# Performance work log

Measured on AMD Instinct MI355X. Metric: run time of the kernel, lower is better.

Reference implementation:

```python
import jax, jax.numpy as jnp
import numpy as np

D_MODEL = 1024
N_HEADS = 16
D_HEAD = 64
D_FF = 4096
BATCH = 4
SEQ = 2048
EPS = 1e-05


def gelu_lean(x):
    cubic = x * x * x
    cdf = 0.5 * (1.0 + jnp.tanh(0.7978845608 * (x + 0.044715 * cubic)))
    return x * cdf


def layernorm(x, gamma, beta):
    mean = jnp.mean(x, axis=-1, keepdims=True)
    var = jnp.mean((x - mean) ** 2, axis=-1, keepdims=True)
    return gamma * ((x - mean) / jnp.sqrt(var + EPS)) + beta


def setup_inputs() -> dict:
    key = jax.random.key(0)
    ks = jax.random.split(key, 8)
    std = 0.02
    return {
        "x": jax.random.normal(ks[0], (BATCH, SEQ, D_MODEL), dtype=jnp.float32),
        "gamma1": jnp.ones((D_MODEL,), jnp.float32),
        "beta1": jnp.zeros((D_MODEL,), jnp.float32),
        "wq": std * jax.random.normal(ks[1], (N_HEADS, D_HEAD, D_MODEL), dtype=jnp.float32),
        "wk": std * jax.random.normal(ks[2], (N_HEADS, D_HEAD, D_MODEL), dtype=jnp.float32),
        "wv": std * jax.random.normal(ks[3], (N_HEADS, D_HEAD, D_MODEL), dtype=jnp.float32),
        "wo": std * jax.random.normal(ks[4], (D_MODEL, N_HEADS * D_HEAD), dtype=jnp.float32),
        "gamma2": jnp.ones((D_MODEL,), jnp.float32),
        "beta2": jnp.zeros((D_MODEL,), jnp.float32),
        "mlp_fc1": std * jax.random.normal(ks[5], (D_FF, D_MODEL), dtype=jnp.float32),
        "mlp_fc2": std * jax.random.normal(ks[6], (D_MODEL, D_FF), dtype=jnp.float32),
    }


def reference(x, gamma1, beta1, wq, wk, wv, wo, gamma2, beta2, mlp_fc1, mlp_fc2):
    n = layernorm(x, gamma1, beta1)  # [B,S,D]
    scale = jnp.sqrt(jnp.float32(D_HEAD))
    # per-head projections, vectorized over heads: [B,S,H,dh]
    q = jnp.einsum("bsd,hed->bshe", n, wq)
    k = jnp.einsum("bsd,hed->bshe", n, wk)
    v = jnp.einsum("bsd,hed->bshe", n, wv)
    scores = jnp.einsum("bqhe,bkhe->bhqk", q, k) / scale  # [B,H,S,S]
    seq = x.shape[1]
    mask = jnp.triu(jnp.ones((seq, seq), dtype=bool), k=1)
    scores = jnp.where(mask, jnp.float32(-1e9), scores)
    weights = jax.nn.softmax(scores, axis=-1)
    attn = jnp.einsum("bhqk,bkhe->bqhe", weights, v)  # [B,S,H,dh]
    concat = attn.reshape(x.shape[0], seq, N_HEADS * D_HEAD)  # head-order concat
    attn_out = concat @ wo.T
    x_resid = x + attn_out
    n2 = layernorm(x_resid, gamma2, beta2)
    hidden = gelu_lean(n2 @ mlp_fc1.T)
    mlp_out = hidden @ mlp_fc2.T
    return x_resid + mlp_out
```

## Files before the change

### kernel.cpp

```cpp
#include <hip/hip_runtime.h>
#include <hip/hip_bf16.h>

#define D_MODEL 1024
#define N_HEADS 16
#define D_HEAD  64
#define D_FF    4096
#define BATCH   4
#define SEQ     2048
#define ROWS    (BATCH*SEQ)
#define LN_EPS  1e-5f

typedef __bf16 bf16;
typedef __bf16 bf16x8 __attribute__((ext_vector_type(8)));
typedef __bf16 bf16x4 __attribute__((ext_vector_type(4)));
typedef float  f32x4  __attribute__((ext_vector_type(4)));

__device__ __forceinline__ void load16_lds(const bf16* g, bf16* l) {
#if defined(__has_builtin) && __has_builtin(__builtin_amdgcn_global_load_lds)
    __builtin_amdgcn_global_load_lds(
        (const __attribute__((address_space(1))) unsigned int*)g,
        (__attribute__((address_space(3))) unsigned int*)l,
        16, 0, 0);
#else
    const int lane = threadIdx.x & 63;
    ((bf16x8*)l)[lane] = *(const bf16x8*)g;
#endif
}

__global__ __launch_bounds__(256) void f2b4_kernel(const float* a, const float* b,
                                                   const float* c, const float* d,
                                                   bf16* oa, bf16* ob, bf16* oc, bf16* od,
                                                   int n) {
    const float* srcs[4] = {a, b, c, d};
    bf16* dsts[4] = {oa, ob, oc, od};
    const float* s = srcs[blockIdx.y];
    bf16* dst = dsts[blockIdx.y];
    int i = blockIdx.x * 256 + threadIdx.x;
    int stride = gridDim.x * 256;
    for (; i < n; i += stride) dst[i] = (bf16)s[i];
}
__global__ __launch_bounds__(256) void f2b2_kernel(const float* a, const float* b,
                                                   bf16* oa, bf16* ob, int n) {
    const float* s = blockIdx.y ? b : a;
    bf16* dst = blockIdx.y ? ob : oa;
    int i = blockIdx.x * 256 + threadIdx.x;
    int stride = gridDim.x * 256;
    for (; i < n; i += stride) dst[i] = (bf16)s[i];
}

__global__ __launch_bounds__(256) void ln_kernel(const float* __restrict__ x,
                                                 const float* __restrict__ gamma,
                                                 const float* __restrict__ beta,
                                                 bf16* __restrict__ out) {
    const int row = blockIdx.x;
    const int tid = threadIdx.x;
    const float* xr = x + (size_t)row * D_MODEL;

    float vals[4];
    float s = 0.f, ss = 0.f;
#pragma unroll
    for (int t = 0; t < 4; ++t) {
        float v = xr[tid + t * 256];
        vals[t] = v;
        s += v;
        ss += v * v;
    }
#pragma unroll
    for (int off = 32; off > 0; off >>= 1) {
        s  += __shfl_xor(s, off, 64);
        ss += __shfl_xor(ss, off, 64);
    }
    __shared__ float sbuf[4], ssbuf[4];
    const int wave = tid >> 6;
    if ((tid & 63) == 0) { sbuf[wave] = s; ssbuf[wave] = ss; }
    __syncthreads();
    s  = sbuf[0] + sbuf[1] + sbuf[2] + sbuf[3];
    ss = ssbuf[0] + ssbuf[1] + ssbuf[2] + ssbuf[3];

    const float mean = s * (1.f / D_MODEL);
    const float var  = ss * (1.f / D_MODEL) - mean * mean;
    const float inv  = rsqrtf(var + LN_EPS);

    bf16* orow = out + (size_t)row * D_MODEL;
#pragma unroll
    for (int t = 0; t < 4; ++t) {
        int c = tid + t * 256;
        orow[c] = (bf16)(gamma[c] * ((vals[t] - mean) * inv) + beta[c]);
    }
}

__device__ __forceinline__ float gelu_f(float x) {
    const float y = x * (0.7978845608f + 0.0356774081f * x * x);
    return x / (1.f + __expf(-2.f * y));
}

template <int EPI, int TN, int BK, int ORD, typename OutT>
__global__ __launch_bounds__(256) void gemm_mt(const bf16* __restrict__ A,
                                               const bf16* __restrict__ W,
                                               OutT* C,
                                               const float* ADD,
                                               bf16* VT,
                                               int M, int N, int K, int LDK) {
    constexpr int WN = TN / 64;
    constexpr int WM = 4 / WN;
    constexpr int SM = (128 / WM) / 16;

    constexpr int AB_ELEMS = 128 * BK + TN * BK;
    constexpr int TB_ELEMS = (EPI == 4) ? 4 * 64 * 72 : 0;
    constexpr int SMEM_ELEMS = AB_ELEMS > TB_ELEMS ? AB_ELEMS : TB_ELEMS;
    __shared__ __align__(16) bf16 smem[SMEM_ELEMS];
    bf16* sA   = smem;
    bf16* sB   = smem + 128 * BK;
    bf16* tbuf = smem;

    const int wave = threadIdx.x >> 6;
    const int lane = threadIdx.x & 63;
    const int quad = lane >> 4;
    const int l16  = lane & 15;
    const int wm   = wave / WN;
    const int wn   = wave % WN;

    const int nN  = N / TN;
    const int b   = blockIdx.x;
    const int xcd = b & 7;
    const int j   = b >> 3;
    int bx, band;
    if constexpr (ORD == 0) {
        bx   = j % nN;
        band = (j / nN) * 8 + xcd;
    } else {
        const int BPX = (M / 128) >> 3;
        bx   = j / BPX;
        band = (j % BPX) * 8 + xcd;
    }

    const int m0 = band * 128;
    const int n0 = bx * TN;

    f32x4 acc[SM][4] = {};

    if constexpr (BK == 32) {
        const int srow = lane >> 2;
        const int scol = (lane & 3) * 8;
        const bf16* gA0 = A + (size_t)(m0 + wave * 32 + srow) * LDK + scol;
        const bf16* gA1 = gA0 + (size_t)16 * LDK;
        bf16* lA0 = &sA[(wave * 32) * 32];
        bf16* lA1 = &sA[(wave * 32 + 16) * 32];
        const bf16* gB0 = W + (size_t)(n0 + wave * (TN / 4) + srow) * LDK + scol;
        const bf16* gB1 = gB0 + (size_t)16 * LDK;
        bf16* lB0 = &sB[(wave * (TN / 4)) * 32];
        bf16* lB1 = &sB[(wave * (TN / 4) + 16) * 32];

        for (int k0 = 0; k0 < K; k0 += 32) {
            load16_lds(gA0 + k0, lA0);
            load16_lds(gA1 + k0, lA1);
            load16_lds(gB0 + k0, lB0);
            if constexpr (TN == 128) load16_lds(gB1 + k0, lB1);
            __syncthreads();

            bf16x8 af[SM], bfr[4];
#pragma unroll
            for (int s = 0; s < SM; ++s)
                af[s] = *reinterpret_cast<const bf16x8*>(&sA[(wm * (128 / WM) + s * 16 + l16) * 32 + quad * 8]);
#pragma unroll
            for (int t = 0; t < 4; ++t)
                bfr[t] = *reinterpret_cast<const bf16x8*>(&sB[(wn * 64 + t * 16 + l16) * 32 + quad * 8]);
#pragma unroll
            for (int s = 0; s < SM; ++s)
#pragma unroll
                for (int t = 0; t < 4; ++t)
                    acc[s][t] = __builtin_amdgcn_mfma_f32_16x16x32_bf16(af[s], bfr[t], acc[s][t], 0, 0, 0);
            __syncthreads();
        }
    } else {
        const int lrow = lane >> 3;
        const int lch  = ((lane & 7) ^ lrow) * 8;
        const bf16* gA = A + (size_t)(m0 + wave * 32 + lrow) * LDK + lch;
        bf16* lA = &sA[(wave * 32) * 64];
        const bf16* gB = W + (size_t)(n0 + wave * (TN / 4) + lrow) * LDK + lch;
        bf16* lB = &sB[(wave * (TN / 4)) * 64];

        for (int k0 = 0; k0 < K; k0 += 64) {
#pragma unroll
            for (int i = 0; i < 4; ++i)
                load16_lds(gA + k0 + (size_t)(8 * i) * LDK, lA + 8 * i * 64);
#pragma unroll
            for (int i = 0; i < (TN / 4) / 8; ++i)
                load16_lds(gB + k0 + (size_t)(8 * i) * LDK, lB + 8 * i * 64);
            __syncthreads();

#pragma unroll
            for (int kk = 0; kk < 2; ++kk) {
                bf16x8 af[SM], bfr[4];
#pragma unroll
                for (int s = 0; s < SM; ++s) {
                    const int row = wm * (128 / WM) + s * 16 + l16;
                    const int sl  = (kk * 4 + quad) ^ (row & 7);
                    af[s] = *reinterpret_cast<const bf16x8*>(&sA[row * 64 + sl * 8]);
                }
#pragma unroll
                for (int t = 0; t < 4; ++t) {
                    const int row = wn * 64 + t * 16 + l16;
                    const int sl  = (kk * 4 + quad) ^ (row & 7);
                    bfr[t] = *reinterpret_cast<const bf16x8*>(&sB[row * 64 + sl * 8]);
                }
#pragma unroll
                for (int s = 0; s < SM; ++s)
#pragma unroll
                    for (int t = 0; t < 4; ++t)
                        acc[s][t] = __builtin_amdgcn_mfma_f32_16x16x32_bf16(af[s], bfr[t], acc[s][t], 0, 0, 0);
            }
            __syncthreads();
        }
    }

    if constexpr (EPI == 4) {
        if (n0 >= 2048) {
            bf16* tw = &tbuf[wave * 64 * 72];
#pragma unroll
            for (int s = 0; s < SM; ++s)
#pragma unroll
                for (int t = 0; t < 4; ++t)
#pragma unroll
                    for (int r = 0; r < 4; ++r)
                        tw[(t * 16 + l16) * 72 + s * 16 + quad * 4 + r] = (bf16)acc[s][t][r];
#pragma unroll
            for (int i = 0; i < 8; ++i) {
                const int flat = i * 64 + lane;
                const int nl = flat >> 3;
                const int mc = flat & 7;
                bf16x8 v = *reinterpret_cast<const bf16x8*>(&tw[nl * 72 + mc * 8]);
                const int vcol = n0 - 2048 + wn * 64 + nl;
                const int m_glob = m0 + wm * 64 + mc * 8;
                const int bb = m_glob >> 11, sp = m_glob & (SEQ - 1);
                const int hh = vcol >> 6,  dh = vcol & 63;
                const size_t tidx = (((size_t)(bb * N_HEADS + hh) * D_HEAD + dh) << 11) + sp;
                *reinterpret_cast<bf16x8*>(&VT[tidx]) = v;
            }
        } else {
            const float qscale = (n0 < 1024) ? 0.125f : 1.0f;
#pragma unroll
            for (int s = 0; s < SM; ++s) {
                const int mbase = m0 + wm * (128 / WM) + s * 16 + quad * 4;
#pragma unroll
                for (int t = 0; t < 4; ++t) {
                    const int n = n0 + wn * 64 + t * 16 + l16;
#pragma unroll
                    for (int r = 0; r < 4; ++r)
                        C[(size_t)(mbase + r) * 2048 + n] = (OutT)(acc[s][t][r] * qscale);
                }
            }
        }
    } else {
#pragma unroll
        for (int s = 0; s < SM; ++s) {
            const int mbase = m0 + wm * (128 / WM) + s * 16 + quad * 4;
#pragma unroll
            for (int t = 0; t < 4; ++t) {
                const int n = n0 + wn * 64 + t * 16 + l16;
#pragma unroll
                for (int r = 0; r < 4; ++r) {
                    float v = acc[s][t][r];
                    if (EPI == 1) v = gelu_f(v);
                    const size_t idx = (size_t)(mbase + r) * N + n;
                    if (EPI == 2) v += ADD[idx];
                    C[idx] = (OutT)v;
                }
            }
        }
    }
}

__global__ __launch_bounds__(256) void flash_attn_kernel(const bf16* __restrict__ qk,
                                                         const bf16* __restrict__ vt,
                                                         bf16* __restrict__ o) {
    const int id   = blockIdx.x;
    const int bhl  = id & 7;
    const int rest = id >> 3;
    const int pair = rest & 15;
    const int bhh  = rest >> 4;
    const int bh   = bhh * 8 + bhl;
    const int b    = bh >> 4;
    const int h    = bh & 15;
    const int wave = threadIdx.x >> 6;
    const int lane = threadIdx.x & 63;
    const int quad = lane >> 4;
    const int l16  = lane & 15;

    __shared__ __align__(16) bf16 sK[2][64 * 64];
    __shared__ __align__(16) bf16 sV[2][64 * 64];

    const bf16* kbase = qk + (size_t)(b * SEQ) * 2048 + 1024 + h * D_HEAD;
    const bf16* vbase = vt + ((size_t)(bh * D_HEAD) << 11);

    const int lrow   = lane >> 3;
    const int lchunk = (lane & 7) ^ lrow;
    const int xr     = l16 & 7;

    auto sig = [](int i) { return (i & 32) + (((i >> 2) & 3) << 3) + (((i >> 4) & 1) << 2) + (i & 3); };
    const int sg0 = sig(wave * 16 + lrow);
    const int sg1 = sig(wave * 16 + 8 + lrow);

    auto stage = [&](int j0, int buf) {
        const bf16* gk0 = kbase + (size_t)(j0 + sg0) * 2048 + lchunk * 8;
        const bf16* gk1 = kbase + (size_t)(j0 + sg1) * 2048 + lchunk * 8;
        const bf16* gv  = vbase + (size_t)(wave * 16 + lrow) * 2048 + j0 + lchunk * 8;
        load16_lds(gk0, &sK[buf][(wave * 16) * 64]);
        load16_lds(gk1, &sK[buf][(wave * 16 + 8) * 64]);
        load16_lds(gv,            &sV[buf][(wave * 16) * 64]);
        load16_lds(gv + 8 * 2048, &sV[buf][(wave * 16 + 8) * 64]);
    };

    for (int half = 0; half < 2; ++half) {
        const int qtile = half ? 31 - pair : pair;
        const int q0 = qtile * 64 + wave * 16;
        const int qg = q0 + l16;
        const size_t qrow = (size_t)(b * SEQ + qg) * 2048 + h * D_HEAD;
        bf16x8 qf0 = *reinterpret_cast<const bf16x8*>(qk + qrow + quad * 8);
        bf16x8 qf1 = *reinterpret_cast<const bf16x8*>(qk + qrow + 32 + quad * 8);

        f32x4 o_acc[4] = {(f32x4)(0.f), (f32x4)(0.f), (f32x4)(0.f), (f32x4)(0.f)};
        float m_q = -1e30f;
        float l_r = 0.f;

        stage(0, 0);
        __syncthreads();

        for (int jt = 0; jt <= qtile; ++jt) {
            const int j0 = jt * 64;
            const int cur = jt & 1;
            if (jt < qtile) stage(j0 + 64, cur ^ 1);

            const bf16* sKc = sK[cur];
            const bf16* sVc = sV[cur];

            f32x4 s_acc[4] = {(f32x4)(0.f), (f32x4)(0.f), (f32x4)(0.f), (f32x4)(0.f)};
            __builtin_amdgcn_s_setprio(1);
#pragma unroll
            for (int nb = 0; nb < 4; ++nb) {
                const int row = nb * 16 + l16;
                const int slot = quad ^ xr;
                bf16x8 kf0 = *reinterpret_cast<const bf16x8*>(&sKc[row * 64 + slot * 8]);
                bf16x8 kf1 = *reinterpret_cast<const bf16x8*>(&sKc[row * 64 + (slot ^ 4) * 8]);
                s_acc[nb] = __builtin_amdgcn_mfma_f32_16x16x32_bf16(kf0, qf0, s_acc[nb], 0, 0, 0);
                s_acc[nb] = __builtin_amdgcn_mfma_f32_16x16x32_bf16(kf1, qf1, s_acc[nb], 0, 0, 0);
            }
            __builtin_amdgcn_s_setprio(0);

            const bool diag = (jt == qtile);
            float p[4][4];
            float mx = -1e30f;
#pragma unroll
            for (int nb = 0; nb < 4; ++nb) {
#pragma unroll
                for (int r = 0; r < 4; ++r) {
                    float s = s_acc[nb][r];
                    if (diag) {
                        const int key = j0 + ((nb & 2) << 4) + (quad << 3) + ((nb & 1) << 2) + r;
                        if (key > qg) s = -1e30f;
                    }
                    p[nb][r] = s;
                    mx = fmaxf(mx, s);
                }
            }
            mx = fmaxf(mx, __shfl_xor(mx, 16, 64));
            mx = fmaxf(mx, __shfl_xor(mx, 32, 64));

            if (!__all(mx <= m_q + 8.0f)) {
                const float mn = fmaxf(m_q, mx);
                const float alpha = __expf(m_q - mn);
                m_q = mn;
                l_r *= alpha;
#pragma unroll
                for (int nb = 0; nb < 4; ++nb) o_acc[nb] *= alpha;
            }

            float ts = 0.f;
#pragma unroll
            for (int nb = 0; nb < 4; ++nb)
#pragma unroll
                for (int r = 0; r < 4; ++r) {
                    const float e = __expf(p[nb][r] - m_q);
                    p[nb][r] = e;
                    ts += e;
                }
            ts += __shfl_xor(ts, 16, 64);
            ts += __shfl_xor(ts, 32, 64);
            l_r += ts;

            bf16x8 pb0, pb1;
#pragma unroll
            for (int r = 0; r < 4; ++r) {
                pb0[r]     = (bf16)p[0][r];
                pb0[4 + r] = (bf16)p[1][r];
                pb1[r]     = (bf16)p[2][r];
                pb1[4 + r] = (bf16)p[3][r];
            }

            __builtin_amdgcn_s_setprio(1);
#pragma unroll
            for (int nb = 0; nb < 4; ++nb) {
                const int row = nb * 16 + l16;
                const int slot = quad ^ xr;
                bf16x8 vf0 = *reinterpret_cast<const bf16x8*>(&sVc[row * 64 + slot * 8]);
                bf16x8 vf1 = *reinterpret_cast<const bf16x8*>(&sVc[row * 64 + (slot ^ 4) * 8]);
                o_acc[nb] = __builtin_amdgcn_mfma_f32_16x16x32_bf16(vf0, pb0, o_acc[nb], 0, 0, 0);
                o_acc[nb] = __builtin_amdgcn_mfma_f32_16x16x32_bf16(vf1, pb1, o_acc[nb], 0, 0, 0);
            }
            __builtin_amdgcn_s_setprio(0);
            __syncthreads();
        }

        const float inv = 1.f / l_r;
#pragma unroll
        for (int nb = 0; nb < 4; ++nb) {
            bf16x4 ov;
#pragma unroll
            for (int r = 0; r < 4; ++r) ov[r] = (bf16)(o_acc[nb][r] * inv);
            *reinterpret_cast<bf16x4*>(
                &o[(size_t)(b * SEQ + qg) * D_MODEL + h * D_HEAD + nb * 16 + quad * 4]) = ov;
        }
    }
}

extern "C" void kernel_launch(void* const* d_in, const int* in_sizes, int n_in,
                              void* d_out, int out_size, void* d_ws, size_t ws_size,
                              hipStream_t stream) {
    const float* x      = (const float*)d_in[0];
    const float* gamma1 = (const float*)d_in[1];
    const float* beta1  = (const float*)d_in[2];
    const float* wq     = (const float*)d_in[3];
    const float* wk     = (const float*)d_in[4];
    const float* wv     = (const float*)d_in[5];
    const float* wo     = (const float*)d_in[6];
    const float* gamma2 = (const float*)d_in[7];
    const float* beta2  = (const float*)d_in[8];
    const float* fc1    = (const float*)d_in[9];
    const float* fc2    = (const float*)d_in[10];
    float* out = (float*)d_out;

    const size_t WSMALL = (size_t)N_HEADS * D_HEAD * D_MODEL;
    const size_t WFF    = (size_t)D_FF * D_MODEL;
    const size_t RD     = (size_t)ROWS * D_MODEL;

    char* wsb = (char*)d_ws;
    bf16* wq_b  = (bf16*)(wsb);
    bf16* wk_b  = wq_b + WSMALL;
    bf16* wv_b  = wk_b + WSMALL;
    bf16* wo_b  = wv_b + WSMALL;
    bf16* fc1_b = wo_b + WSMALL;
    bf16* fc2_b = fc1_b + WFF;
    bf16* slotA = fc2_b + WFF;
    bf16* qkb   = slotA + RD;
    bf16* vtb   = qkb + 2 * RD;

    bf16* n1    = slotA;
    bf16* attnb = slotA;
    bf16* hid   = slotA;
    float* resid = out;

    const size_t need_single = (size_t)(24 + 64 + 16) * 1024 * 1024;
    const bool single = ws_size >= need_single;
    bf16* n2 = single ? (bf16*)(wsb + (size_t)88 * 1024 * 1024) : vtb;

    f2b4_kernel<<<dim3(64, 4), 256, 0, stream>>>(wq, wk, wv, wo, wq_b, wk_b, wv_b, wo_b, (int)WSMALL);
    f2b2_kernel<<<dim3(256, 2), 256, 0, stream>>>(fc1, fc2, fc1_b, fc2_b, (int)WFF);

    ln_kernel<<<ROWS, 256, 0, stream>>>(x, gamma1, beta1, n1);
    gemm_mt<4, 128, 64, 1, bf16><<<(3072 / 128) * (ROWS / 128), 256, 0, stream>>>(n1, wq_b, qkb, nullptr, vtb, ROWS, 3072, D_MODEL, D_MODEL);
    flash_attn_kernel<<<1024, 256, 0, stream>>>(qkb, vtb, attnb);
    gemm_mt<2, 64, 64, 0, float><<<(D_MODEL / 64) * (ROWS / 128), 256, 0, stream>>>(attnb, wo_b, resid, x, nullptr, ROWS, D_MODEL, D_MODEL, D_MODEL);
    ln_kernel<<<ROWS, 256, 0, stream>>>(resid, gamma2, beta2, n2);

    if (single) {
        gemm_mt<1, 128, 64, 1, bf16><<<(D_FF / 128) * (ROWS / 128), 256, 0, stream>>>(n2, fc1_b, hid, nullptr, nullptr, ROWS, D_FF, D_MODEL, D_MODEL);
        gemm_mt<2, 64, 64, 0, float><<<(D_MODEL / 64) * (ROWS / 128), 256, 0, stream>>>(hid, fc2_b, out, resid, nullptr, ROWS, D_MODEL, D_FF, D_FF);
    } else {
        const int CHUNK = 4096;
        for (int c = 0; c < ROWS / CHUNK; ++c) {
            const bf16*  n2c    = n2    + (size_t)c * CHUNK * D_MODEL;
            const float* residc = resid + (size_t)c * CHUNK * D_MODEL;
            float*       outc   = out   + (size_t)c * CHUNK * D_MODEL;
            gemm_mt<1, 128, 64, 1, bf16><<<(D_FF / 128) * (CHUNK / 128), 256, 0, stream>>>(n2c, fc1_b, hid, nullptr, nullptr, CHUNK, D_FF, D_MODEL, D_MODEL);
            gemm_mt<2, 64, 64, 0, float><<<(D_MODEL / 64) * (CHUNK / 128), 256, 0, stream>>>(hid, fc2_b, outc, residc, nullptr, CHUNK, D_MODEL, D_FF, D_FF);
        }
    }
}
```

Baseline: 499.5 us.

## Double-buffer LDS tiles in BK=64 GEMM path to overlap loads with MFMA

For non-EPI-4 GEMMs with BK=64, the kernel now allocates two LDS buffers. It issues the global-to-LDS loads for the next K tile before computing on the current one, so memory latency overlaps with MFMA work, and it drops one barrier per iteration. The cost is doubled shared memory per block, which can reduce occupancy. Correctness relies on the single barrier after compute also covering completion of the async global_load_lds writes.

```diff
diff --git a/kernel.cpp b/kernel.cpp
--- a/kernel.cpp
+++ b/kernel.cpp
@@ -105,7 +105,9 @@
     constexpr int WM = 4 / WN;
     constexpr int SM = (128 / WM) / 16;
 
-    constexpr int AB_ELEMS = 128 * BK + TN * BK;
+    constexpr bool PP = (EPI != 4) && (BK == 64);
+    constexpr int BUFE = 128 * BK + TN * BK;
+    constexpr int AB_ELEMS = (PP ? 2 : 1) * BUFE;
     constexpr int TB_ELEMS = (EPI == 4) ? 4 * 64 * 72 : 0;
     constexpr int SMEM_ELEMS = AB_ELEMS > TB_ELEMS ? AB_ELEMS : TB_ELEMS;
     __shared__ __align__(16) bf16 smem[SMEM_ELEMS];
@@ -176,19 +178,21 @@
         const int lrow = lane >> 3;
         const int lch  = ((lane & 7) ^ lrow) * 8;
         const bf16* gA = A + (size_t)(m0 + wave * 32 + lrow) * LDK + lch;
-        bf16* lA = &sA[(wave * 32) * 64];
         const bf16* gB = W + (size_t)(n0 + wave * (TN / 4) + lrow) * LDK + lch;
-        bf16* lB = &sB[(wave * (TN / 4)) * 64];
-
-        for (int k0 = 0; k0 < K; k0 += 64) {
+
+        auto stageg = [&](int k0, int buf) {
+            bf16* lA = smem + buf * BUFE + (wave * 32) * 64;
+            bf16* lB = smem + buf * BUFE + 128 * BK + (wave * (TN / 4)) * 64;
 #pragma unroll
             for (int i = 0; i < 4; ++i)
                 load16_lds(gA + k0 + (size_t)(8 * i) * LDK, lA + 8 * i * 64);
 #pragma unroll
             for (int i = 0; i < (TN / 4) / 8; ++i)
                 load16_lds(gB + k0 + (size_t)(8 * i) * LDK, lB + 8 * i * 64);
-            __syncthreads();
-
+        };
+        auto comp = [&](int buf) {
+            const bf16* cA = smem + buf * BUFE;
+            const bf16* cB = cA + 128 * BK;
 #pragma unroll
             for (int kk = 0; kk < 2; ++kk) {
                 bf16x8 af[SM], bfr[4];
@@ -196,13 +200,13 @@
                 for (int s = 0; s < SM; ++s) {
                     const int row = wm * (128 / WM) + s * 16 + l16;
                     const int sl  = (kk * 4 + quad) ^ (row & 7);
-                    af[s] = *reinterpret_cast<const bf16x8*>(&sA[row * 64 + sl * 8]);
+                    af[s] = *reinterpret_cast<const bf16x8*>(&cA[row * 64 + sl * 8]);
                 }
 #pragma unroll
                 for (int t = 0; t < 4; ++t) {
                     const int row = wn * 64 + t * 16 + l16;
                     const int sl  = (kk * 4 + quad) ^ (row & 7);
-                    bfr[t] = *reinterpret_cast<const bf16x8*>(&sB[row * 64 + sl * 8]);
+                    bfr[t] = *reinterpret_cast<const bf16x8*>(&cB[row * 64 + sl * 8]);
                 }
 #pragma unroll
                 for (int s = 0; s < SM; ++s)
@@ -210,7 +214,25 @@
                     for (int t = 0; t < 4; ++t)
                         acc[s][t] = __builtin_amdgcn_mfma_f32_16x16x32_bf16(af[s], bfr[t], acc[s][t], 0, 0, 0);
             }
+        };
+
+        if constexpr (PP) {
+            stageg(0, 0);
             __syncthreads();
+            int cur = 0;
+            for (int k0 = 0; k0 < K; k0 += 64) {
+                if (k0 + 64 < K) stageg(k0 + 64, cur ^ 1);
+                comp(cur);
+                __syncthreads();
+                cur ^= 1;
+            }
+        } else {
+            for (int k0 = 0; k0 < K; k0 += 64) {
+                stageg(k0, 0);
+                __syncthreads();
+                comp(0);
+                __syncthreads();
+            }
         }
     }
 
```

New measurement: 513.5 us. 1.03x slower.
